# Optimization experiments

Measured on AMD Instinct MI355X. Metric: run time of the kernel, lower is better.

## Reference

```python
import jax, jax.numpy as jnp
import numpy as np

ORDER = 3  # cubic B-splines, matching BSpline(..., 3)


def bspline_basis(x, t, order):
    """Cox-de Boor recursion, vectorized over batch and features.

    x: [B, F] evaluation points
    t: [F, M] sorted knot vectors (M = num_basis + order + 1)
    returns: [B, F, M-1-order] basis values B_j^{order}(x), zero outside the
    base interval [t[order], t[M-1-order]] (scipy extrapolate=False + nan_to_num).
    """
    M = t.shape[-1]
    xd = x[:, :, None]            # [B, F, 1]
    tb = t[None, :, :]            # [1, F, M]
    # degree-0 indicator functions: [B, F, M-1]
    B = ((xd >= tb[:, :, :-1]) & (xd < tb[:, :, 1:])).astype(x.dtype)
    for d in range(1, order + 1):
        t0 = tb[:, :, : M - d - 1]   # t_j
        td = tb[:, :, d : M - 1]     # t_{j+d}
        t1 = tb[:, :, 1 : M - d]     # t_{j+1}
        td1 = tb[:, :, d + 1 : M]    # t_{j+d+1}
        den1 = td - t0
        den2 = td1 - t1
        w1 = jnp.where(den1 > 0, (xd - t0) / jnp.where(den1 > 0, den1, 1.0), 0.0)
        w2 = jnp.where(den2 > 0, (td1 - xd) / jnp.where(den2 > 0, den2, 1.0), 0.0)
        B = w1 * B[:, :, : M - d - 1] + w2 * B[:, :, 1 : M - d]
    # zero outside the base interval [t[order], t[n]] (scipy NaN -> nan_to_num -> 0)
    lo = t[None, :, order]           # [1, F]
    hi = t[None, :, M - 1 - order]   # [1, F]
    valid = ((x >= lo) & (x <= hi)).astype(x.dtype)  # [B, F]
    return B * valid[:, :, None]


def setup_inputs() -> dict:
    key = jax.random.key(0)
    k_x, k_w, k_b = jax.random.split(key, 3)
    batch, in_features, out_features, num_basis = 4096, 512, 512, 30
    x = jax.random.normal(k_x, (batch, in_features), dtype=jnp.float32)
    knots = jnp.broadcast_to(
        jnp.linspace(-2.0, 2.0, num_basis + ORDER + 1, dtype=jnp.float32),
        (in_features, num_basis + ORDER + 1),
    )
    weights = jax.random.normal(k_w, (out_features, in_features, num_basis), dtype=jnp.float32)
    bias = jax.random.normal(k_b, (out_features,), dtype=jnp.float32)
    return {"x": x, "knots": knots, "weights": weights, "bias": bias}


def reference(x, knots, weights, bias):
    ks = jnp.sort(knots, axis=-1)              # module sorts knots before eval
    basis = bspline_basis(x, ks, ORDER)        # [B, F, num_basis]
    out = jnp.einsum("bij,kij->bk", basis, weights)
    return out + bias
```

## Files before the change

### kernel.cpp

```cpp
#include <hip/hip_runtime.h>
#include <hip/hip_bf16.h>
#include <stdint.h>


#define BATCH 4096
#define INF   512
#define OUTF  512
#define NB    30
#define NBP   32
#define NKNOT 34
#define KDIMP (INF * NBP)

#define BM 128
#define BN 128
#define BK 64
#define KSPLIT 4
#define KCHUNK (KDIMP / KSPLIT)
#define NT     (KCHUNK / BK)

typedef short v8s __attribute__((ext_vector_type(8)));
typedef float v4f __attribute__((ext_vector_type(4)));

__device__ __forceinline__ unsigned short f2bf(float f) {
  uint32_t u = __float_as_uint(f);
  uint32_t r = (u + 0x7fffu + ((u >> 16) & 1u)) >> 16;
  return (unsigned short)r;
}

__device__ __forceinline__ void gload16(const unsigned short* g, unsigned short* l) {
  auto gp = reinterpret_cast<const __attribute__((address_space(1))) unsigned short*>(
      reinterpret_cast<uintptr_t>(g));
  auto lp = reinterpret_cast<__attribute__((address_space(3))) unsigned short*>(
      reinterpret_cast<uintptr_t>(l));
  __builtin_amdgcn_global_load_lds(gp, lp, 16, 0, 0);
}

__global__ __launch_bounds__(256) void w_cast_kernel(const float* __restrict__ in,
                                                     unsigned short* __restrict__ out) {
  int idx = blockIdx.x * 256 + threadIdx.x;
  int k   = idx >> 13;
  int rem = idx & 8191;
  int i   = rem >> 4;
  int jp  = rem & 15;
  int j   = jp * 2;
  const float* src = in + ((size_t)k * INF + i) * NB;
  float lo = (j     < NB) ? src[j]     : 0.f;
  float hi = (j + 1 < NB) ? src[j + 1] : 0.f;
  ((uint32_t*)out)[idx] = (uint32_t)f2bf(lo) | ((uint32_t)f2bf(hi) << 16);
}

__global__ __launch_bounds__(256) void xt_kernel(const float* __restrict__ x,
                                                 float* __restrict__ xT) {
  __shared__ float tile[32][33];
  int b0 = blockIdx.x * 32;
  int f0 = blockIdx.y * 32;
  int lx = threadIdx.x & 31;
  int ly = threadIdx.x >> 5;
  #pragma unroll
  for (int q = 0; q < 4; ++q)
    tile[ly + q * 8][lx] = x[(size_t)(b0 + ly + q * 8) * INF + f0 + lx];
  __syncthreads();
  #pragma unroll
  for (int q = 0; q < 4; ++q)
    xT[(size_t)(f0 + ly + q * 8) * BATCH + b0 + lx] = tile[lx][ly + q * 8];
}

__global__ __launch_bounds__(256) void bias_kernel(const float* __restrict__ bias,
                                                   float* __restrict__ out) {
  int idx = blockIdx.x * 256 + threadIdx.x;
  out[idx] = bias[idx & (OUTF - 1)];
}

__device__ __forceinline__ void evalA(unsigned short* Abuf, int b, int hf,
                                      float xv, const float* __restrict__ tk) {
  unsigned rowb = (unsigned)b * 128;
  unsigned x7   = (unsigned)(b & 7);
  char* base = (char*)Abuf;
  uint4 z = {0u, 0u, 0u, 0u};
  #pragma unroll
  for (int s = 0; s < 4; ++s) {
    unsigned slot = ((unsigned)(hf * 4 + s)) ^ x7;
    *(uint4*)(base + rowb + (slot << 4)) = z;
  }
  float tlo = tk[3], thi = tk[30];
  if (!(xv >= tlo && xv <= thi)) return;
  float t0v = tk[0];
  float h   = tk[1] - t0v;
  int m = (int)floorf((xv - t0v) * __builtin_amdgcn_rcpf(h));
  m = m < 3 ? 3 : (m > 30 ? 30 : m);
  while (m > 3 && xv < tk[m]) --m;
  while (m < 30 && xv >= tk[m + 1]) ++m;
  float Nv[4], left[4], right[4];
  Nv[0] = 1.f;
  #pragma unroll
  for (int d = 1; d <= 3; ++d) {
    left[d]  = xv - tk[m + 1 - d];
    right[d] = tk[m + d] - xv;
    float saved = 0.f;
    #pragma unroll
    for (int r = 0; r < d; ++r) {
      float temp = Nv[r] * __builtin_amdgcn_rcpf(right[r + 1] + left[d - r]);
      Nv[r] = saved + right[r + 1] * temp;
      saved = left[d - r] * temp;
    }
    Nv[d] = saved;
  }
  int j0 = m - 3;
  int d0 = (hf * 16) + (j0 >> 1);
  #define WR32(d, v) { unsigned by = (unsigned)(d) * 4u; \
    *(uint32_t*)(base + rowb + ((((by >> 4) ^ x7) << 4) | (by & 15u))) = (v); }
  if (j0 & 1) {
    WR32(d0,     (uint32_t)f2bf(Nv[0]) << 16);
    WR32(d0 + 1, (uint32_t)f2bf(Nv[1]) | ((uint32_t)f2bf(Nv[2]) << 16));
    WR32(d0 + 2, (uint32_t)f2bf(Nv[3]));
  } else {
    WR32(d0,     (uint32_t)f2bf(Nv[0]) | ((uint32_t)f2bf(Nv[1]) << 16));
    WR32(d0 + 1, (uint32_t)f2bf(Nv[2]) | ((uint32_t)f2bf(Nv[3]) << 16));
  }
  #undef WR32
}

__global__ __launch_bounds__(256, 2) void gemm_kernel(const float* __restrict__ xT,
                                                      const float* __restrict__ knots,
                                                      const unsigned short* __restrict__ Bt,
                                                      float* __restrict__ C) {
  __shared__ unsigned short As[2][BM * BK];
  __shared__ unsigned short Bs[2][BN * BK];
  int tid  = threadIdx.x;
  int lane = tid & 63;
  int w    = tid >> 6;

  int bid = blockIdx.x;
  int swz = (bid & 7) * 64 + (bid >> 3);
  int bn  = swz >> 7;
  int rem = swz & 127;
  int bm  = rem >> 2;
  int ks  = rem & 3;

  int row0 = bm * BM;
  int col0 = bn * BN;
  int kk0  = ks * KCHUNK;
  int fbase = kk0 / NBP;

  int eb = tid & 127;
  int hf = tid >> 7;

  int lrow = lane >> 3;
  int lseg = (lane & 7) ^ lrow;
  const unsigned short* gb = Bt + (size_t)(col0 + w * 8 + lrow) * KDIMP + kk0 + lseg * 8;
  unsigned short* lBbase[2] = { &Bs[0][w * 512], &Bs[1][w * 512] };

  v4f acc[4][4];
  #pragma unroll
  for (int i = 0; i < 4; ++i)
    #pragma unroll
    for (int j = 0; j < 4; ++j)
      acc[i][j] = (v4f){0.f, 0.f, 0.f, 0.f};

  int wr  = (w >> 1) & 1;
  int wc  = w & 1;
  int r16 = lane & 15;
  int kg  = lane >> 4;
  unsigned s0   = ((unsigned)kg ^ (unsigned)(r16 & 7)) << 4;
  unsigned aoff = (unsigned)(wr * 64 + r16) * 128;
  unsigned boff = (unsigned)(wc * 64 + r16) * 128;

  float xv_s = xT[(size_t)(fbase + hf) * BATCH + row0 + eb];
  {
    #pragma unroll
    for (int q = 0; q < 4; ++q)
      gload16(gb + (size_t)q * (32 * KDIMP), lBbase[0] + q * 2048);
    evalA(As[0], eb, hf, xv_s, knots + (size_t)(fbase + hf) * NKNOT);
  }
  xv_s = xT[(size_t)(fbase + 2 + hf) * BATCH + row0 + eb];
  __syncthreads();

  for (int t = 0; t < NT; ++t) {
    int c = t & 1;
    if (t + 1 < NT) {
      const unsigned short* src = gb + (size_t)(t + 1) * BK;
      #pragma unroll
      for (int q = 0; q < 4; ++q)
        gload16(src + (size_t)q * (32 * KDIMP), lBbase[c ^ 1] + q * 2048);
      int f = fbase + 2 * (t + 1) + hf;
      evalA(As[c ^ 1], eb, hf, xv_s, knots + (size_t)f * NKNOT);
    }
    float xv_n = 0.f;
    if (t + 2 < NT)
      xv_n = xT[(size_t)(fbase + 2 * (t + 2) + hf) * BATCH + row0 + eb];

    const char* Ab = (const char*)As[c];
    const char* Bb = (const char*)Bs[c];
    #pragma unroll
    for (int kc = 0; kc < 2; ++kc) {
      unsigned sk = s0 ^ (unsigned)(kc << 6);
      v8s af[4], bf[4];
      #pragma unroll
      for (int mi = 0; mi < 4; ++mi)
        af[mi] = *(const v8s*)(Ab + aoff + mi * 2048 + sk);
      #pragma unroll
      for (int ni = 0; ni < 4; ++ni)
        bf[ni] = *(const v8s*)(Bb + boff + ni * 2048 + sk);
      #pragma unroll
      for (int mi = 0; mi < 4; ++mi)
        #pragma unroll
        for (int ni = 0; ni < 4; ++ni)
          acc[mi][ni] = __builtin_amdgcn_mfma_f32_16x16x32_bf16(af[mi], bf[ni], acc[mi][ni], 0, 0, 0);
    }
    __syncthreads();
    xv_s = xv_n;
  }

  int crow = (lane >> 4) * 4;
  int ccol = lane & 15;
  #pragma unroll
  for (int mi = 0; mi < 4; ++mi) {
    #pragma unroll
    for (int ni = 0; ni < 4; ++ni) {
      int r = row0 + wr * 64 + mi * 16 + crow;
      int c = col0 + wc * 64 + ni * 16 + ccol;
      #pragma unroll
      for (int q = 0; q < 4; ++q)
        atomicAdd(&C[(size_t)(r + q) * OUTF + c], acc[mi][ni][q]);
    }
  }
}

extern "C" void kernel_launch(void* const* d_in, const int* in_sizes, int n_in,
                              void* d_out, int out_size, void* d_ws, size_t ws_size,
                              hipStream_t stream) {
  const float* x     = (const float*)d_in[0];
  const float* knots = (const float*)d_in[1];
  const float* W     = (const float*)d_in[2];
  const float* bias  = (const float*)d_in[3];
  float* out = (float*)d_out;

  unsigned short* Wt = (unsigned short*)d_ws;
  float*          xT = (float*)((char*)d_ws + (size_t)OUTF * KDIMP * 2);

  w_cast_kernel<<<(OUTF * KDIMP / 2) / 256, 256, 0, stream>>>(W, Wt);
  xt_kernel<<<dim3(BATCH / 32, INF / 32), 256, 0, stream>>>(x, xT);
  bias_kernel<<<(BATCH * OUTF) / 256, 256, 0, stream>>>(bias, out);
  gemm_kernel<<<(BATCH / BM) * (OUTF / BN) * KSPLIT, 256, 0, stream>>>(xT, knots, Wt, out);
}
```

Baseline: 232.7 us.

## Precompute spline basis in separate kernel, single-buffer GEMM with higher occupancy

Moves the B-spline evaluation out of the GEMM main loop into the transpose kernel, which now writes packed bf16 basis values and the span index per (feature, batch). The GEMM drops LDS double buffering for a single buffer with two barriers per step, raises launch bounds to 4 blocks per SU, and doubles the K split to 8. This removes per-tile ALU work and LDS pressure from the GEMM so more waves can hide latency. In exchange it adds extra global traffic for the precomputed basis, exposes load latency without double buffering, and doubles the atomic output traffic.

```diff
diff --git a/kernel.cpp b/kernel.cpp
--- a/kernel.cpp
+++ b/kernel.cpp
@@ -14,9 +14,10 @@
 #define BM 128
 #define BN 128
 #define BK 64
-#define KSPLIT 4
+#define KSPLIT 8
 #define KCHUNK (KDIMP / KSPLIT)
 #define NT     (KCHUNK / BK)
+#define FPC    (KCHUNK / NBP)
 
 typedef short v8s __attribute__((ext_vector_type(8)));
 typedef float v4f __attribute__((ext_vector_type(4)));
@@ -49,8 +50,10 @@
   ((uint32_t*)out)[idx] = (uint32_t)f2bf(lo) | ((uint32_t)f2bf(hi) << 16);
 }
 
-__global__ __launch_bounds__(256) void xt_kernel(const float* __restrict__ x,
-                                                 float* __restrict__ xT) {
+__global__ __launch_bounds__(256) void basis_kernel(const float* __restrict__ x,
+                                                    const float* __restrict__ knots,
+                                                    uint2* __restrict__ valsT,
+                                                    unsigned char* __restrict__ j0T) {
   __shared__ float tile[32][33];
   int b0 = blockIdx.x * 32;
   int f0 = blockIdx.y * 32;
@@ -61,8 +64,43 @@
     tile[ly + q * 8][lx] = x[(size_t)(b0 + ly + q * 8) * INF + f0 + lx];
   __syncthreads();
   #pragma unroll
-  for (int q = 0; q < 4; ++q)
-    xT[(size_t)(f0 + ly + q * 8) * BATCH + b0 + lx] = tile[lx][ly + q * 8];
+  for (int q = 0; q < 4; ++q) {
+    int fy = ly + q * 8;
+    float xv = tile[lx][fy];
+    const float* tk = knots + (size_t)(f0 + fy) * NKNOT;
+    uint2 pv = {0u, 0u};
+    int j0 = 0;
+    float tlo = tk[3], thi = tk[30];
+    if (xv >= tlo && xv <= thi) {
+      float t0v = tk[0];
+      float h   = tk[1] - t0v;
+      int m = (int)floorf((xv - t0v) * __builtin_amdgcn_rcpf(h));
+      m = m < 3 ? 3 : (m > 30 ? 30 : m);
+      while (m > 3 && xv < tk[m]) --m;
+      while (m < 30 && xv >= tk[m + 1]) ++m;
+      float Nv[4], left[4], right[4];
+      Nv[0] = 1.f;
+      #pragma unroll
+      for (int d = 1; d <= 3; ++d) {
+        left[d]  = xv - tk[m + 1 - d];
+        right[d] = tk[m + d] - xv;
+        float saved = 0.f;
+        #pragma unroll
+        for (int r = 0; r < d; ++r) {
+          float temp = Nv[r] * __builtin_amdgcn_rcpf(right[r + 1] + left[d - r]);
+          Nv[r] = saved + right[r + 1] * temp;
+          saved = left[d - r] * temp;
+        }
+        Nv[d] = saved;
+      }
+      j0 = m - 3;
+      pv.x = (uint32_t)f2bf(Nv[0]) | ((uint32_t)f2bf(Nv[1]) << 16);
+      pv.y = (uint32_t)f2bf(Nv[2]) | ((uint32_t)f2bf(Nv[3]) << 16);
+    }
+    size_t oi = (size_t)(f0 + fy) * BATCH + b0 + lx;
+    valsT[oi] = pv;
+    j0T[oi]   = (unsigned char)j0;
+  }
 }
 
 __global__ __launch_bounds__(256) void bias_kernel(const float* __restrict__ bias,
@@ -71,10 +109,10 @@
   out[idx] = bias[idx & (OUTF - 1)];
 }
 
-__device__ __forceinline__ void evalA(unsigned short* Abuf, int b, int hf,
-                                      float xv, const float* __restrict__ tk) {
-  unsigned rowb = (unsigned)b * 128;
-  unsigned x7   = (unsigned)(b & 7);
+__device__ __forceinline__ void writeA(unsigned short* Abuf, int eb, int hf,
+                                       uint2 v, int j0) {
+  unsigned rowb = (unsigned)eb * 128;
+  unsigned x7   = (unsigned)(eb & 7);
   char* base = (char*)Abuf;
   uint4 z = {0u, 0u, 0u, 0u};
   #pragma unroll
@@ -82,73 +120,50 @@
     unsigned slot = ((unsigned)(hf * 4 + s)) ^ x7;
     *(uint4*)(base + rowb + (slot << 4)) = z;
   }
-  float tlo = tk[3], thi = tk[30];
-  if (!(xv >= tlo && xv <= thi)) return;
-  float t0v = tk[0];
-  float h   = tk[1] - t0v;
-  int m = (int)floorf((xv - t0v) * __builtin_amdgcn_rcpf(h));
-  m = m < 3 ? 3 : (m > 30 ? 30 : m);
-  while (m > 3 && xv < tk[m]) --m;
-  while (m < 30 && xv >= tk[m + 1]) ++m;
-  float Nv[4], left[4], right[4];
-  Nv[0] = 1.f;
-  #pragma unroll
-  for (int d = 1; d <= 3; ++d) {
-    left[d]  = xv - tk[m + 1 - d];
-    right[d] = tk[m + d] - xv;
-    float saved = 0.f;
-    #pragma unroll
-    for (int r = 0; r < d; ++r) {
-      float temp = Nv[r] * __builtin_amdgcn_rcpf(right[r + 1] + left[d - r]);
-      Nv[r] = saved + right[r + 1] * temp;
-      saved = left[d - r] * temp;
-    }
-    Nv[d] = saved;
-  }
-  int j0 = m - 3;
-  int d0 = (hf * 16) + (j0 >> 1);
-  #define WR32(d, v) { unsigned by = (unsigned)(d) * 4u; \
-    *(uint32_t*)(base + rowb + ((((by >> 4) ^ x7) << 4) | (by & 15u))) = (v); }
+  int d0 = hf * 16 + (j0 >> 1);
+  #define WR32(d, val) { unsigned by = (unsigned)(d) * 4u; \
+    *(uint32_t*)(base + rowb + ((((by >> 4) ^ x7) << 4) | (by & 15u))) = (val); }
   if (j0 & 1) {
-    WR32(d0,     (uint32_t)f2bf(Nv[0]) << 16);
-    WR32(d0 + 1, (uint32_t)f2bf(Nv[1]) | ((uint32_t)f2bf(Nv[2]) << 16));
-    WR32(d0 + 2, (uint32_t)f2bf(Nv[3]));
+    WR32(d0,     v.x << 16);
+    WR32(d0 + 1, (v.x >> 16) | (v.y << 16));
+    WR32(d0 + 2, v.y >> 16);
   } else {
-    WR32(d0,     (uint32_t)f2bf(Nv[0]) | ((uint32_t)f2bf(Nv[1]) << 16));
-    WR32(d0 + 1, (uint32_t)f2bf(Nv[2]) | ((uint32_t)f2bf(Nv[3]) << 16));
+    WR32(d0,     v.x);
+    WR32(d0 + 1, v.y);
   }
   #undef WR32
 }
 
-__global__ __launch_bounds__(256, 2) void gemm_kernel(const float* __restrict__ xT,
-                                                      const float* __restrict__ knots,
+__global__ __launch_bounds__(256, 4) void gemm_kernel(const uint2* __restrict__ valsT,
+                                                      const unsigned char* __restrict__ j0T,
                                                       const unsigned short* __restrict__ Bt,
                                                       float* __restrict__ C) {
-  __shared__ unsigned short As[2][BM * BK];
-  __shared__ unsigned short Bs[2][BN * BK];
+  __shared__ unsigned short As[BM * BK];
+  __shared__ unsigned short Bs[BN * BK];
   int tid  = threadIdx.x;
   int lane = tid & 63;
   int w    = tid >> 6;
 
   int bid = blockIdx.x;
-  int swz = (bid & 7) * 64 + (bid >> 3);
-  int bn  = swz >> 7;
-  int rem = swz & 127;
-  int bm  = rem >> 2;
-  int ks  = rem & 3;
+  int swz = (bid & 7) * 128 + (bid >> 3);
+  int bn  = swz >> 8;
+  int rem = swz & 255;
+  int ks  = rem >> 5;
+  int bm  = rem & 31;
 
   int row0 = bm * BM;
   int col0 = bn * BN;
   int kk0  = ks * KCHUNK;
-  int fbase = kk0 / NBP;
+  int fbase = ks * FPC;
 
   int eb = tid & 127;
   int hf = tid >> 7;
+  size_t vidx0 = (size_t)(fbase + hf) * BATCH + row0 + eb;
 
   int lrow = lane >> 3;
   int lseg = (lane & 7) ^ lrow;
   const unsigned short* gb = Bt + (size_t)(col0 + w * 8 + lrow) * KDIMP + kk0 + lseg * 8;
-  unsigned short* lBbase[2] = { &Bs[0][w * 512], &Bs[1][w * 512] };
+  unsigned short* lB = &Bs[w * 512];
 
   v4f acc[4][4];
   #pragma unroll
@@ -165,32 +180,26 @@
   unsigned aoff = (unsigned)(wr * 64 + r16) * 128;
   unsigned boff = (unsigned)(wc * 64 + r16) * 128;
 
-  float xv_s = xT[(size_t)(fbase + hf) * BATCH + row0 + eb];
-  {
-    #pragma unroll
-    for (int q = 0; q < 4; ++q)
-      gload16(gb + (size_t)q * (32 * KDIMP), lBbase[0] + q * 2048);
-    evalA(As[0], eb, hf, xv_s, knots + (size_t)(fbase + hf) * NKNOT);
-  }
-  xv_s = xT[(size_t)(fbase + 2 + hf) * BATCH + row0 + eb];
+  uint2 vc = valsT[vidx0];
+  int   jc = j0T[vidx0];
+  writeA(As, eb, hf, vc, jc);
+  #pragma unroll
+  for (int q = 0; q < 4; ++q)
+    gload16(gb + (size_t)q * (32 * KDIMP), lB + q * 2048);
+  uint2 vn = valsT[vidx0 + 8192];
+  int   jn = j0T[vidx0 + 8192];
   __syncthreads();
 
   for (int t = 0; t < NT; ++t) {
-    int c = t & 1;
-    if (t + 1 < NT) {
-      const unsigned short* src = gb + (size_t)(t + 1) * BK;
-      #pragma unroll
-      for (int q = 0; q < 4; ++q)
-        gload16(src + (size_t)q * (32 * KDIMP), lBbase[c ^ 1] + q * 2048);
-      int f = fbase + 2 * (t + 1) + hf;
-      evalA(As[c ^ 1], eb, hf, xv_s, knots + (size_t)f * NKNOT);
-    }
-    float xv_n = 0.f;
-    if (t + 2 < NT)
-      xv_n = xT[(size_t)(fbase + 2 * (t + 2) + hf) * BATCH + row0 + eb];
-
-    const char* Ab = (const char*)As[c];
-    const char* Bb = (const char*)Bs[c];
+    uint2 v2 = {0u, 0u};
+    int   j2 = 0;
+    if (t + 2 < NT) {
+      size_t ix = vidx0 + (size_t)(t + 2) * 8192;
+      v2 = valsT[ix];
+      j2 = j0T[ix];
+    }
+    const char* Ab = (const char*)As;
+    const char* Bb = (const char*)Bs;
     #pragma unroll
     for (int kc = 0; kc < 2; ++kc) {
       unsigned sk = s0 ^ (unsigned)(kc << 6);
@@ -208,7 +217,15 @@
           acc[mi][ni] = __builtin_amdgcn_mfma_f32_16x16x32_bf16(af[mi], bf[ni], acc[mi][ni], 0, 0, 0);
     }
     __syncthreads();
-    xv_s = xv_n;
+    if (t + 1 < NT) {
+      writeA(As, eb, hf, vn, jn);
+      const unsigned short* src = gb + (size_t)(t + 1) * BK;
+      #pragma unroll
+      for (int q = 0; q < 4; ++q)
+        gload16(src + (size_t)q * (32 * KDIMP), lB + q * 2048);
+      vn = v2; jn = j2;
+      __syncthreads();
+    }
   }
 
   int crow = (lane >> 4) * 4;
@@ -235,11 +252,13 @@
   const float* bias  = (const float*)d_in[3];
   float* out = (float*)d_out;
 
-  unsigned short* Wt = (unsigned short*)d_ws;
-  float*          xT = (float*)((char*)d_ws + (size_t)OUTF * KDIMP * 2);
+  unsigned short* Wt    = (unsigned short*)d_ws;
+  uint2*          valsT = (uint2*)((char*)d_ws + (size_t)OUTF * KDIMP * 2);
+  unsigned char*  j0T   = (unsigned char*)((char*)d_ws + (size_t)OUTF * KDIMP * 2
+                                           + (size_t)INF * BATCH * 8);
 
   w_cast_kernel<<<(OUTF * KDIMP / 2) / 256, 256, 0, stream>>>(W, Wt);
-  xt_kernel<<<dim3(BATCH / 32, INF / 32), 256, 0, stream>>>(x, xT);
+  basis_kernel<<<dim3(BATCH / 32, INF / 32), 256, 0, stream>>>(x, knots, valsT, j0T);
   bias_kernel<<<(BATCH * OUTF) / 256, 256, 0, stream>>>(bias, out);
-  gemm_kernel<<<(BATCH / BM) * (OUTF / BN) * KSPLIT, 256, 0, stream>>>(xT, knots, Wt, out);
-}
+  gemm_kernel<<<(BATCH / BM) * (OUTF / BN) * KSPLIT, 256, 0, stream>>>(valsT, j0T, Wt, out);
+}
```

After: 197.5 us. -15.1%, faster.
